# Kernel optimization log

Hardware: AMD Instinct MI355X
Metric: run time of the kernel (lower is better)

The kernel has to match this reference:

```python
import jax, jax.numpy as jnp
import numpy as np

NUM_HEADS = 16


def setup_inputs() -> dict:
    key = jax.random.key(0)
    k0, k1, k2, k3 = jax.random.split(key, 4)
    B, N, C = 8, 1024, 1024
    D = C // NUM_HEADS
    x = jax.random.normal(k0, (B, N, C), dtype=jnp.float32)
    # RoPE angle table [1, N, 1, head_dim]
    rope_freqs = jax.random.uniform(k1, (1, N, 1, D), dtype=jnp.float32) * (2.0 * jnp.pi)
    # qkv: Linear(dim, 3*dim, bias=False); proj: Linear(dim, dim) with bias
    qkv_w = jax.random.normal(k2, (3 * C, C), dtype=jnp.float32) * 0.02
    proj_w = jax.random.normal(k3, (C, C), dtype=jnp.float32) * 0.02
    proj_b = jnp.zeros((C,), dtype=jnp.float32)
    return {"x": x, "rope_freqs": rope_freqs, "qkv_w": qkv_w, "proj_w": proj_w, "proj_b": proj_b}


def _rotate_half(t):
    t1, t2 = jnp.split(t, 2, axis=-1)
    return jnp.concatenate([-t2, t1], axis=-1)


def reference(x, rope_freqs, qkv_w, proj_w, proj_b):
    B, N, C = x.shape
    H = NUM_HEADS
    D = C // H
    scale = D ** (-0.5)
    # QKV projection -> [3, B, H, N, D]
    qkv = (x @ qkv_w.T).reshape(B, N, 3, H, D).transpose(2, 0, 3, 1, 4)
    q, k, v = qkv[0], qkv[1], qkv[2]
    # RoPE: freqs [1, N, 1, D] -> [1, 1, N, D], applied to all tokens (n_special = 0)
    freqs = jnp.transpose(rope_freqs, (0, 2, 1, 3))
    cos = jnp.cos(freqs).astype(q.dtype)
    sin = jnp.sin(freqs).astype(q.dtype)
    q = q * cos + _rotate_half(q) * sin
    k = k * cos + _rotate_half(k) * sin
    # Full materialized attention (as in source)
    attn = jax.nn.softmax(jnp.einsum("bhnd,bhmd->bhnm", q, k) * scale, axis=-1)
    out = jnp.einsum("bhnm,bhmd->bhnd", attn, v)  # [B, H, N, D]
    out = out.transpose(0, 2, 1, 3).reshape(B, N, C)
    return out @ proj_w.T + proj_b
```

## Files before the change

kernel.cpp:

```cpp
#include <hip/hip_runtime.h>


typedef __attribute__((ext_vector_type(8))) short bf16x8;
typedef __attribute__((ext_vector_type(4))) float floatx4;
typedef __attribute__((ext_vector_type(4))) unsigned int u32x4;
typedef __attribute__((ext_vector_type(2))) unsigned int u32x2;

__device__ __forceinline__ void gld16(const void* g, void* l) {
  __builtin_amdgcn_global_load_lds((const __attribute__((address_space(1))) void*)g,
                                   (__attribute__((address_space(3))) void*)l, 16, 0, 0);
}

__device__ __forceinline__ short f2bf(float f) {
  unsigned u = __builtin_bit_cast(unsigned, f);
  u = (u + 0x7FFFu + ((u >> 16) & 1u)) >> 16;
  return (short)u;
}
__device__ __forceinline__ unsigned cvtpk(float lo, float hi) {
  unsigned r;
  asm("v_cvt_pk_bf16_f32 %0, %1, %2" : "=v"(r) : "v"(lo), "v"(hi));
  return r;
}
__device__ __forceinline__ float pexp(float x) {
  float r;
  asm("v_exp_f32 %0, %1" : "=v"(r) : "v"(x));
  return r;
}

__global__ __launch_bounds__(256) void prep_all(const float* __restrict__ sx,
                                                const float* __restrict__ sq,
                                                const float* __restrict__ sp,
                                                short* __restrict__ dst,
                                                const float* __restrict__ ropef,
                                                float2* __restrict__ tbl) {
  int bid = blockIdx.x;
  if (bid < 12288) {
    int i = bid * 256 + threadIdx.x;
    const float4* src;
    if (i < 2097152)      src = reinterpret_cast<const float4*>(sx) + i;
    else if (i < 2883584) src = reinterpret_cast<const float4*>(sq) + (i - 2097152);
    else                  src = reinterpret_cast<const float4*>(sp) + (i - 2883584);
    float4 v = *src;
    short4 o;
    o.x = f2bf(v.x); o.y = f2bf(v.y); o.z = f2bf(v.z); o.w = f2bf(v.w);
    reinterpret_cast<short4*>(dst)[i] = o;
  } else {
    int i = (bid - 12288) * 256 + threadIdx.x;
    float v = ropef[i];
    tbl[i] = make_float2(cosf(v), sinf(v));
  }
}

#define QSCALE 0.18033688011112042f

__device__ __forceinline__ void gemm_main(const short* __restrict__ A,
                                          const short* __restrict__ Bm,
                                          short* As, short* Bs,
                                          floatx4 (&acc)[2][4],
                                          int bx, int by) {
  const int tid = threadIdx.x;
  const int wid = tid >> 6, lane = tid & 63;
  const int g = lane >> 4, l15 = lane & 15;
  const int wr = wid >> 2, wc = wid & 3;
  const size_t trow = (size_t)by * 128, tcol = (size_t)bx * 256;
  floatx4 zero = {0.f, 0.f, 0.f, 0.f};
  #pragma unroll
  for (int i = 0; i < 2; ++i)
    #pragma unroll
    for (int j = 0; j < 4; ++j) acc[i][j] = zero;

  auto stage = [&](int buf, int k0) {
    {
      const int cb = wid * 64;
      const int c  = cb + lane;
      const int r  = c >> 3, s = c & 7;
      const int koff = k0 + ((s ^ (r & 7)) << 3);
      gld16(A + (trow + r) * 1024 + koff, As + buf * 8192 + (size_t)cb * 8);
    }
    #pragma unroll
    for (int i = 0; i < 2; ++i) {
      const int cb = (i * 16 + wid) * 64;
      const int c  = cb + lane;
      const int r  = c >> 3, s = c & 7;
      const int koff = k0 + ((s ^ (r & 7)) << 3);
      gld16(Bm + (tcol + r) * 1024 + koff, Bs + buf * 16384 + (size_t)cb * 8);
    }
  };

  stage(0, 0);
  __syncthreads();

  for (int t = 0; t < 16; ++t) {
    const int buf = t & 1;
    if (t < 15) stage(buf ^ 1, (t + 1) * 64);
    const short* Ab = As + buf * 8192;
    const short* Bb = Bs + buf * 16384;
    #pragma unroll
    for (int ks = 0; ks < 2; ++ks) {
      bf16x8 af[2], bfr[4];
      #pragma unroll
      for (int mi = 0; mi < 2; ++mi) {
        int row = wr * 32 + mi * 16 + l15;
        int ch  = (ks * 4 + g) ^ (row & 7);
        af[mi] = *reinterpret_cast<const bf16x8*>(Ab + row * 64 + ch * 8);
      }
      #pragma unroll
      for (int nt = 0; nt < 4; ++nt) {
        int row = wc * 64 + nt * 16 + l15;
        int ch  = (ks * 4 + g) ^ (row & 7);
        bfr[nt] = *reinterpret_cast<const bf16x8*>(Bb + row * 64 + ch * 8);
      }
      __builtin_amdgcn_s_setprio(1);
      #pragma unroll
      for (int mi = 0; mi < 2; ++mi)
        #pragma unroll
        for (int nt = 0; nt < 4; ++nt)
          acc[mi][nt] = __builtin_amdgcn_mfma_f32_16x16x32_bf16(af[mi], bfr[nt],
                                                                acc[mi][nt], 0, 0, 0);
      __builtin_amdgcn_s_setprio(0);
    }
    __syncthreads();
  }
}

__global__ __launch_bounds__(1024, 4) void gemm_qkv_k(const short* __restrict__ A,
                                                      const short* __restrict__ Bm,
                                                      const float2* __restrict__ tbl,
                                                      short* __restrict__ qo,
                                                      short* __restrict__ ko,
                                                      short* __restrict__ vt) {
  extern __shared__ __align__(16) short smem[];
  short* As = smem;
  short* Bs = smem + 16384;
  const int id  = blockIdx.y * 12 + blockIdx.x;
  const int sid = (id & 7) * 96 + (id >> 3);
  const int bx  = sid % 12, by = sid / 12;
  floatx4 acc[2][4];
  gemm_main(A, Bm, As, Bs, acc, bx, by);

  const int tid = threadIdx.x;
  const int wid = tid >> 6, lane = tid & 63;
  const int g = lane >> 4, l15 = lane & 15;
  const int wr = wid >> 2, wc = wid & 3;
  const int trow = by * 128, tcol = bx * 256;
  const int which = bx >> 2;

  if (which < 2) {
    short* dst = which == 0 ? qo : ko;
    const float sc = which == 0 ? QSCALE : 1.0f;
    #pragma unroll
    for (int nt = 0; nt < 2; ++nt) {
      int col = tcol + wc * 64 + nt * 16 + l15;
      int hc = col & 1023, h = hc >> 6, d1 = hc & 63;
      #pragma unroll
      for (int mi = 0; mi < 2; ++mi)
        #pragma unroll
        for (int r = 0; r < 4; ++r) {
          int rowg = trow + wr * 32 + mi * 16 + g * 4 + r;
          int b = rowg >> 10, n = rowg & 1023;
          float a1 = acc[mi][nt][r], a2 = acc[mi][nt + 2][r];
          float2 c1 = tbl[n * 64 + d1];
          float2 c2 = tbl[n * 64 + d1 + 32];
          float o1 = (a1 * c1.x - a2 * c1.y) * sc;
          float o2 = (a2 * c2.x + a1 * c2.y) * sc;
          size_t base = ((size_t)(b * 16 + h) * 1024 + n) * 64;
          dst[base + d1]      = f2bf(o1);
          dst[base + d1 + 32] = f2bf(o2);
        }
    }
  } else {
    #pragma unroll
    for (int nt = 0; nt < 4; ++nt) {
      int col = tcol + wc * 64 + nt * 16 + l15;
      int hc = col & 1023, h = hc >> 6, d = hc & 63;
      #pragma unroll
      for (int mi = 0; mi < 2; ++mi) {
        int rowg = trow + wr * 32 + mi * 16 + g * 4;
        int b = rowg >> 10, n0 = rowg & 1023;
        ushort4 pk;
        pk.x = (unsigned short)f2bf(acc[mi][nt][0]);
        pk.y = (unsigned short)f2bf(acc[mi][nt][1]);
        pk.z = (unsigned short)f2bf(acc[mi][nt][2]);
        pk.w = (unsigned short)f2bf(acc[mi][nt][3]);
        *reinterpret_cast<ushort4*>((unsigned short*)vt +
            ((size_t)(b * 16 + h) * 64 + d) * 1024 + n0) = pk;
      }
    }
  }
}

__global__ __launch_bounds__(1024, 4) void gemm_proj_k(const short* __restrict__ A,
                                                       const short* __restrict__ Bm,
                                                       const float* __restrict__ pb,
                                                       float* __restrict__ out) {
  extern __shared__ __align__(16) short smem[];
  short* As = smem;
  short* Bs = smem + 16384;
  const int id  = blockIdx.y * 4 + blockIdx.x;
  const int sid = (id & 7) * 32 + (id >> 3);
  const int bx  = sid % 4, by = sid / 4;
  floatx4 acc[2][4];
  gemm_main(A, Bm, As, Bs, acc, bx, by);

  const int tid = threadIdx.x;
  const int wid = tid >> 6, lane = tid & 63;
  const int g = lane >> 4, l15 = lane & 15;
  const int wr = wid >> 2, wc = wid & 3;
  const int trow = by * 128, tcol = bx * 256;
  #pragma unroll
  for (int nt = 0; nt < 4; ++nt) {
    int col = tcol + wc * 64 + nt * 16 + l15;
    float bias = pb[col];
    #pragma unroll
    for (int mi = 0; mi < 2; ++mi)
      #pragma unroll
      for (int r = 0; r < 4; ++r) {
        int rowg = trow + wr * 32 + mi * 16 + g * 4 + r;
        out[(size_t)rowg * 1024 + col] = acc[mi][nt][r] + bias;
      }
  }
}

__global__ __launch_bounds__(256) void attn_kernel(const short* __restrict__ qs,
                                                   const short* __restrict__ ksrc,
                                                   const short* __restrict__ vt,
                                                   short* __restrict__ aout) {
  __shared__ __align__(16) short Kl[3][64 * 64];
  __shared__ __align__(16) short Vl[3][64 * 64];

  const int tid = threadIdx.x, wid = tid >> 6, lane = tid & 63;
  const int g = lane >> 4, l15 = lane & 15;
  const int bh = blockIdx.x, q0 = blockIdx.y * 256;
  const size_t bhoff = (size_t)bh * 1024 * 64;
  const short* Kb = ksrc + bhoff;
  const short* Vb = vt + bhoff;
  const int slb = (lane & 48) + ((lane >> 4) << 2);

  const short* QpA = qs + bhoff + (size_t)(q0 + wid * 16 + l15) * 64 + g * 8;
  bf16x8 qA0 = *reinterpret_cast<const bf16x8*>(QpA);
  bf16x8 qA1 = *reinterpret_cast<const bf16x8*>(QpA + 32);
  bf16x8 qB0 = *reinterpret_cast<const bf16x8*>(QpA + 64 * 64);
  bf16x8 qB1 = *reinterpret_cast<const bf16x8*>(QpA + 64 * 64 + 32);
  bf16x8 qC0 = *reinterpret_cast<const bf16x8*>(QpA + 128 * 64);
  bf16x8 qC1 = *reinterpret_cast<const bf16x8*>(QpA + 128 * 64 + 32);
  bf16x8 qD0 = *reinterpret_cast<const bf16x8*>(QpA + 192 * 64);
  bf16x8 qD1 = *reinterpret_cast<const bf16x8*>(QpA + 192 * 64 + 32);

  floatx4 oA[4], oB[4], oC[4], oD[4];
  floatx4 zero = {0.f, 0.f, 0.f, 0.f};
  #pragma unroll
  for (int i = 0; i < 4; ++i) { oA[i] = zero; oB[i] = zero; oC[i] = zero; oD[i] = zero; }
  float lrunA = 0.f, lrunB = 0.f, lrunC = 0.f, lrunD = 0.f;

  auto stage = [&](int buf, int t) {
    #pragma unroll
    for (int i = 0; i < 2; ++i) {
      const int cb = (i * 4 + wid) * 64;
      const int c = cb + lane;
      const int r = c >> 3, s = c & 7;
      const int off = (s ^ (r & 7)) << 3;
      gld16(Kb + (size_t)(t * 64 + r) * 64 + off, &Kl[buf][cb * 8]);
      gld16(Vb + (size_t)r * 1024 + t * 64 + off, &Vl[buf][cb * 8]);
    }
  };

#define SOFTSLICE(s_, lrun, pa)                                                \
  do {                                                                         \
    float p0 = pexp(s_[0][0]), p1 = pexp(s_[0][1]);                            \
    float p2 = pexp(s_[0][2]), p3 = pexp(s_[0][3]);                            \
    float p4 = pexp(s_[1][0]), p5 = pexp(s_[1][1]);                            \
    float p6 = pexp(s_[1][2]), p7 = pexp(s_[1][3]);                            \
    lrun += ((p0 + p1) + (p2 + p3)) + ((p4 + p5) + (p6 + p7));                 \
    unsigned wa0 = cvtpk(p0, p1), wa1 = cvtpk(p2, p3);                         \
    unsigned wb0 = cvtpk(p4, p5), wb1 = cvtpk(p6, p7);                         \
    u32x2 y0 = __builtin_amdgcn_permlane32_swap(wa0, wb0, false, false);       \
    u32x2 z0 = __builtin_amdgcn_permlane16_swap(y0[0], y0[1], false, false);   \
    u32x2 y1 = __builtin_amdgcn_permlane32_swap(wa1, wb1, false, false);       \
    u32x2 z1 = __builtin_amdgcn_permlane16_swap(y1[0], y1[1], false, false);   \
    u32x4 aw = {z0[0], z1[0], z0[1], z1[1]};                                   \
    pa = __builtin_bit_cast(bf16x8, aw);                                       \
  } while (0)

#define QKSLICE(base, sA_, sB_, sC_, sD_)                                      \
  __builtin_amdgcn_s_setprio(1);                                               \
  _Pragma("unroll")                                                            \
  for (int kk = 0; kk < 2; ++kk) {                                             \
    int krow = (base + kk) * 16 + l15;                                         \
    int ch0 = (g ^ (krow & 7)) << 3, ch1 = ((4 + g) ^ (krow & 7)) << 3;        \
    bf16x8 kf0 = *reinterpret_cast<const bf16x8*>(&Kl[btop][krow * 64 + ch0]); \
    sA_[kk] = __builtin_amdgcn_mfma_f32_16x16x32_bf16(kf0, qA0, sA_[kk],0,0,0);\
    sB_[kk] = __builtin_amdgcn_mfma_f32_16x16x32_bf16(kf0, qB0, sB_[kk],0,0,0);\
    sC_[kk] = __builtin_amdgcn_mfma_f32_16x16x32_bf16(kf0, qC0, sC_[kk],0,0,0);\
    sD_[kk] = __builtin_amdgcn_mfma_f32_16x16x32_bf16(kf0, qD0, sD_[kk],0,0,0);\
    bf16x8 kf1 = *reinterpret_cast<const bf16x8*>(&Kl[btop][krow * 64 + ch1]); \
    sA_[kk] = __builtin_amdgcn_mfma_f32_16x16x32_bf16(kf1, qA1, sA_[kk],0,0,0);\
    sB_[kk] = __builtin_amdgcn_mfma_f32_16x16x32_bf16(kf1, qB1, sB_[kk],0,0,0);\
    sC_[kk] = __builtin_amdgcn_mfma_f32_16x16x32_bf16(kf1, qC1, sC_[kk],0,0,0);\
    sD_[kk] = __builtin_amdgcn_mfma_f32_16x16x32_bf16(kf1, qD1, sD_[kk],0,0,0);\
  }                                                                            \
  __builtin_amdgcn_s_setprio(0);

#define PVSLICE(chsel, paA_, paB_, paC_, paD_)                                 \
  __builtin_amdgcn_s_setprio(1);                                               \
  _Pragma("unroll")                                                            \
  for (int nt = 0; nt < 4; ++nt) {                                             \
    int row = nt * 16 + l15;                                                   \
    int ch = (((chsel) + g) ^ (row & 7)) << 3;                                 \
    bf16x8 vf = *reinterpret_cast<const bf16x8*>(&Vl[btop][row * 64 + ch]);    \
    oA[nt] = __builtin_amdgcn_mfma_f32_16x16x32_bf16(paA_, vf, oA[nt],0,0,0);  \
    oB[nt] = __builtin_amdgcn_mfma_f32_16x16x32_bf16(paB_, vf, oB[nt],0,0,0);  \
    oC[nt] = __builtin_amdgcn_mfma_f32_16x16x32_bf16(paC_, vf, oC[nt],0,0,0);  \
    oD[nt] = __builtin_amdgcn_mfma_f32_16x16x32_bf16(paD_, vf, oD[nt],0,0,0);  \
  }                                                                            \
  __builtin_amdgcn_s_setprio(0);

  stage(0, 0);
  stage(1, 1);
  asm volatile("s_waitcnt vmcnt(4)" ::: "memory");
  __builtin_amdgcn_s_barrier();
  asm volatile("" ::: "memory");

  int btop = 0;
  for (int t = 0; t < 16; ++t) {
    if (t < 14) {
      int bnx = btop + 2; if (bnx >= 3) bnx -= 3;
      stage(bnx, t + 2);
    }

    {
      floatx4 sA[2], sB[2], sC[2], sD[2];
      #pragma unroll
      for (int kk = 0; kk < 2; ++kk) { sA[kk]=zero; sB[kk]=zero; sC[kk]=zero; sD[kk]=zero; }
      QKSLICE(0, sA, sB, sC, sD);
      bf16x8 paA, paB, paC, paD;
      SOFTSLICE(sA, lrunA, paA);
      SOFTSLICE(sB, lrunB, paB);
      SOFTSLICE(sC, lrunC, paC);
      SOFTSLICE(sD, lrunD, paD);
      PVSLICE(0, paA, paB, paC, paD);
    }
    {
      floatx4 sA[2], sB[2], sC[2], sD[2];
      #pragma unroll
      for (int kk = 0; kk < 2; ++kk) { sA[kk]=zero; sB[kk]=zero; sC[kk]=zero; sD[kk]=zero; }
      QKSLICE(2, sA, sB, sC, sD);
      bf16x8 paA, paB, paC, paD;
      SOFTSLICE(sA, lrunA, paA);
      SOFTSLICE(sB, lrunB, paB);
      SOFTSLICE(sC, lrunC, paC);
      SOFTSLICE(sD, lrunD, paD);
      PVSLICE(4, paA, paB, paC, paD);
    }

    if (t < 15) {
      if (t < 14) asm volatile("s_waitcnt vmcnt(4)" ::: "memory");
      else        asm volatile("s_waitcnt vmcnt(0)" ::: "memory");
      __builtin_amdgcn_s_barrier();
      asm volatile("" ::: "memory");
    }
    btop = btop + 1 == 3 ? 0 : btop + 1;
  }

  const int b = bh >> 4, h = bh & 15;
  lrunA += __shfl_xor(lrunA, 16); lrunA += __shfl_xor(lrunA, 32);
  lrunB += __shfl_xor(lrunB, 16); lrunB += __shfl_xor(lrunB, 32);
  lrunC += __shfl_xor(lrunC, 16); lrunC += __shfl_xor(lrunC, 32);
  lrunD += __shfl_xor(lrunD, 16); lrunD += __shfl_xor(lrunD, 32);
  float invA = 1.f / lrunA, invB = 1.f / lrunB;
  float invC = 1.f / lrunC, invD = 1.f / lrunD;
  #pragma unroll
  for (int r = 0; r < 4; ++r) {
    float irA = __shfl(invA, slb + r);
    float irB = __shfl(invB, slb + r);
    float irC = __shfl(invC, slb + r);
    float irD = __shfl(invD, slb + r);
    int nA = q0 + wid * 16 + g * 4 + r;
    size_t baseA = ((size_t)(b * 1024) + nA) * 1024 + h * 64;
    size_t baseB = baseA + (size_t)64 * 1024;
    size_t baseC = baseA + (size_t)128 * 1024;
    size_t baseD = baseA + (size_t)192 * 1024;
    #pragma unroll
    for (int nt = 0; nt < 4; ++nt) {
      aout[baseA + nt * 16 + l15] = f2bf(oA[nt][r] * irA);
      aout[baseB + nt * 16 + l15] = f2bf(oB[nt][r] * irB);
      aout[baseC + nt * 16 + l15] = f2bf(oC[nt][r] * irC);
      aout[baseD + nt * 16 + l15] = f2bf(oD[nt][r] * irD);
    }
  }
#undef SOFTSLICE
#undef QKSLICE
#undef PVSLICE
}

extern "C" void kernel_launch(void* const* d_in, const int* in_sizes, int n_in,
                              void* d_out, int out_size, void* d_ws, size_t ws_size,
                              hipStream_t stream) {
  const float* x      = (const float*)d_in[0];
  const float* ropef  = (const float*)d_in[1];
  const float* qkv_w  = (const float*)d_in[2];
  const float* proj_w = (const float*)d_in[3];
  const float* proj_b = (const float*)d_in[4];
  float* out = (float*)d_out;

  char* ws = (char*)d_ws;
  short*  xb  = (short*)(ws + 0);
  short*  wqb = (short*)(ws + 16777216);
  short*  wpb = (short*)(ws + 23068672);
  short*  qb  = (short*)(ws + 25165824);
  short*  kb  = (short*)(ws + 41943040);
  short*  vtb = (short*)(ws + 58720256);
  short*  aob = (short*)(ws + 75497472);
  float2* tbl = (float2*)(ws + 92274688);

  prep_all<<<12544, 256, 0, stream>>>(x, qkv_w, proj_w, xb, ropef, tbl);

  gemm_qkv_k<<<dim3(12, 64), 1024, 98304, stream>>>(xb, wqb, tbl, qb, kb, vtb);
  attn_kernel<<<dim3(128, 4), 256, 0, stream>>>(qb, kb, vtb, aob);
  gemm_proj_k<<<dim3(4, 64), 1024, 98304, stream>>>(aob, wpb, proj_b, out);
}
```

Baseline: 156.1 us.

## Triple-buffer GEMM k-loop with 512-thread blocks and larger per-wave tiles

The shared GEMM mainloop moves from double to triple buffering, prefetching two k-stages ahead and replacing __syncthreads with explicit vmcnt waits plus s_barrier. Blocks shrink from 1024 to 512 threads, so each wave computes a 64x64 subtile with 16 accumulators instead of 8, and LDS grows to 144KB. The fp32-to-bf16 prep kernel becomes grid-stride with packed v_cvt_pk_bf16 conversions. The aim is better latency hiding and more operand reuse per wave, at the cost of more registers and LDS, which may reduce occupancy.

```diff
diff --git a/kernel.cpp b/kernel.cpp
--- a/kernel.cpp
+++ b/kernel.cpp
@@ -34,18 +34,20 @@
                                                 const float* __restrict__ ropef,
                                                 float2* __restrict__ tbl) {
   int bid = blockIdx.x;
-  if (bid < 12288) {
-    int i = bid * 256 + threadIdx.x;
-    const float4* src;
-    if (i < 2097152)      src = reinterpret_cast<const float4*>(sx) + i;
-    else if (i < 2883584) src = reinterpret_cast<const float4*>(sq) + (i - 2097152);
-    else                  src = reinterpret_cast<const float4*>(sp) + (i - 2883584);
-    float4 v = *src;
-    short4 o;
-    o.x = f2bf(v.x); o.y = f2bf(v.y); o.z = f2bf(v.z); o.w = f2bf(v.w);
-    reinterpret_cast<short4*>(dst)[i] = o;
+  if (bid < 2048) {
+    for (int i = bid * 256 + threadIdx.x; i < 3145728; i += 2048 * 256) {
+      const float4* src;
+      if (i < 2097152)      src = reinterpret_cast<const float4*>(sx) + i;
+      else if (i < 2883584) src = reinterpret_cast<const float4*>(sq) + (i - 2097152);
+      else                  src = reinterpret_cast<const float4*>(sp) + (i - 2883584);
+      float4 v = *src;
+      uint2 o;
+      o.x = cvtpk(v.x, v.y);
+      o.y = cvtpk(v.z, v.w);
+      reinterpret_cast<uint2*>(dst)[i] = o;
+    }
   } else {
-    int i = (bid - 12288) * 256 + threadIdx.x;
+    int i = (bid - 2048) * 256 + threadIdx.x;
     float v = ropef[i];
     tbl[i] = make_float2(cosf(v), sinf(v));
   }
@@ -56,7 +58,7 @@
 __device__ __forceinline__ void gemm_main(const short* __restrict__ A,
                                           const short* __restrict__ Bm,
                                           short* As, short* Bs,
-                                          floatx4 (&acc)[2][4],
+                                          floatx4 (&acc)[4][4],
                                           int bx, int by) {
   const int tid = threadIdx.x;
   const int wid = tid >> 6, lane = tid & 63;
@@ -65,21 +67,22 @@
   const size_t trow = (size_t)by * 128, tcol = (size_t)bx * 256;
   floatx4 zero = {0.f, 0.f, 0.f, 0.f};
   #pragma unroll
-  for (int i = 0; i < 2; ++i)
+  for (int i = 0; i < 4; ++i)
     #pragma unroll
     for (int j = 0; j < 4; ++j) acc[i][j] = zero;
 
   auto stage = [&](int buf, int k0) {
-    {
-      const int cb = wid * 64;
+    #pragma unroll
+    for (int i = 0; i < 2; ++i) {
+      const int cb = (i * 8 + wid) * 64;
       const int c  = cb + lane;
       const int r  = c >> 3, s = c & 7;
       const int koff = k0 + ((s ^ (r & 7)) << 3);
       gld16(A + (trow + r) * 1024 + koff, As + buf * 8192 + (size_t)cb * 8);
     }
     #pragma unroll
-    for (int i = 0; i < 2; ++i) {
-      const int cb = (i * 16 + wid) * 64;
+    for (int i = 0; i < 4; ++i) {
+      const int cb = (i * 8 + wid) * 64;
       const int c  = cb + lane;
       const int r  = c >> 3, s = c & 7;
       const int koff = k0 + ((s ^ (r & 7)) << 3);
@@ -88,19 +91,25 @@
   };
 
   stage(0, 0);
-  __syncthreads();
-
+  stage(1, 64);
+  asm volatile("s_waitcnt vmcnt(6)" ::: "memory");
+  __builtin_amdgcn_s_barrier();
+  asm volatile("" ::: "memory");
+
+  int btop = 0;
   for (int t = 0; t < 16; ++t) {
-    const int buf = t & 1;
-    if (t < 15) stage(buf ^ 1, (t + 1) * 64);
-    const short* Ab = As + buf * 8192;
-    const short* Bb = Bs + buf * 16384;
+    if (t < 14) {
+      int bnx = btop + 2; if (bnx >= 3) bnx -= 3;
+      stage(bnx, (t + 2) * 64);
+    }
+    const short* Ab = As + btop * 8192;
+    const short* Bb = Bs + btop * 16384;
     #pragma unroll
     for (int ks = 0; ks < 2; ++ks) {
-      bf16x8 af[2], bfr[4];
-      #pragma unroll
-      for (int mi = 0; mi < 2; ++mi) {
-        int row = wr * 32 + mi * 16 + l15;
+      bf16x8 af[4], bfr[4];
+      #pragma unroll
+      for (int mi = 0; mi < 4; ++mi) {
+        int row = wr * 64 + mi * 16 + l15;
         int ch  = (ks * 4 + g) ^ (row & 7);
         af[mi] = *reinterpret_cast<const bf16x8*>(Ab + row * 64 + ch * 8);
       }
@@ -112,30 +121,36 @@
       }
       __builtin_amdgcn_s_setprio(1);
       #pragma unroll
-      for (int mi = 0; mi < 2; ++mi)
+      for (int mi = 0; mi < 4; ++mi)
         #pragma unroll
         for (int nt = 0; nt < 4; ++nt)
           acc[mi][nt] = __builtin_amdgcn_mfma_f32_16x16x32_bf16(af[mi], bfr[nt],
                                                                 acc[mi][nt], 0, 0, 0);
       __builtin_amdgcn_s_setprio(0);
     }
-    __syncthreads();
-  }
-}
-
-__global__ __launch_bounds__(1024, 4) void gemm_qkv_k(const short* __restrict__ A,
-                                                      const short* __restrict__ Bm,
-                                                      const float2* __restrict__ tbl,
-                                                      short* __restrict__ qo,
-                                                      short* __restrict__ ko,
-                                                      short* __restrict__ vt) {
+    if (t < 15) {
+      if (t < 14) asm volatile("s_waitcnt vmcnt(6)" ::: "memory");
+      else        asm volatile("s_waitcnt vmcnt(0)" ::: "memory");
+      __builtin_amdgcn_s_barrier();
+      asm volatile("" ::: "memory");
+    }
+    btop = btop + 1 == 3 ? 0 : btop + 1;
+  }
+}
+
+__global__ __launch_bounds__(512) void gemm_qkv_k(const short* __restrict__ A,
+                                                  const short* __restrict__ Bm,
+                                                  const float2* __restrict__ tbl,
+                                                  short* __restrict__ qo,
+                                                  short* __restrict__ ko,
+                                                  short* __restrict__ vt) {
   extern __shared__ __align__(16) short smem[];
   short* As = smem;
-  short* Bs = smem + 16384;
+  short* Bs = smem + 24576;
   const int id  = blockIdx.y * 12 + blockIdx.x;
   const int sid = (id & 7) * 96 + (id >> 3);
   const int bx  = sid % 12, by = sid / 12;
-  floatx4 acc[2][4];
+  floatx4 acc[4][4];
   gemm_main(A, Bm, As, Bs, acc, bx, by);
 
   const int tid = threadIdx.x;
@@ -153,10 +168,10 @@
       int col = tcol + wc * 64 + nt * 16 + l15;
       int hc = col & 1023, h = hc >> 6, d1 = hc & 63;
       #pragma unroll
-      for (int mi = 0; mi < 2; ++mi)
+      for (int mi = 0; mi < 4; ++mi)
         #pragma unroll
         for (int r = 0; r < 4; ++r) {
-          int rowg = trow + wr * 32 + mi * 16 + g * 4 + r;
+          int rowg = trow + wr * 64 + mi * 16 + g * 4 + r;
           int b = rowg >> 10, n = rowg & 1023;
           float a1 = acc[mi][nt][r], a2 = acc[mi][nt + 2][r];
           float2 c1 = tbl[n * 64 + d1];
@@ -174,8 +189,8 @@
       int col = tcol + wc * 64 + nt * 16 + l15;
       int hc = col & 1023, h = hc >> 6, d = hc & 63;
       #pragma unroll
-      for (int mi = 0; mi < 2; ++mi) {
-        int rowg = trow + wr * 32 + mi * 16 + g * 4;
+      for (int mi = 0; mi < 4; ++mi) {
+        int rowg = trow + wr * 64 + mi * 16 + g * 4;
         int b = rowg >> 10, n0 = rowg & 1023;
         ushort4 pk;
         pk.x = (unsigned short)f2bf(acc[mi][nt][0]);
@@ -189,17 +204,17 @@
   }
 }
 
-__global__ __launch_bounds__(1024, 4) void gemm_proj_k(const short* __restrict__ A,
-                                                       const short* __restrict__ Bm,
-                                                       const float* __restrict__ pb,
-                                                       float* __restrict__ out) {
+__global__ __launch_bounds__(512) void gemm_proj_k(const short* __restrict__ A,
+                                                   const short* __restrict__ Bm,
+                                                   const float* __restrict__ pb,
+                                                   float* __restrict__ out) {
   extern __shared__ __align__(16) short smem[];
   short* As = smem;
-  short* Bs = smem + 16384;
+  short* Bs = smem + 24576;
   const int id  = blockIdx.y * 4 + blockIdx.x;
   const int sid = (id & 7) * 32 + (id >> 3);
   const int bx  = sid % 4, by = sid / 4;
-  floatx4 acc[2][4];
+  floatx4 acc[4][4];
   gemm_main(A, Bm, As, Bs, acc, bx, by);
 
   const int tid = threadIdx.x;
@@ -212,10 +227,10 @@
     int col = tcol + wc * 64 + nt * 16 + l15;
     float bias = pb[col];
     #pragma unroll
-    for (int mi = 0; mi < 2; ++mi)
+    for (int mi = 0; mi < 4; ++mi)
       #pragma unroll
       for (int r = 0; r < 4; ++r) {
-        int rowg = trow + wr * 32 + mi * 16 + g * 4 + r;
+        int rowg = trow + wr * 64 + mi * 16 + g * 4 + r;
         out[(size_t)rowg * 1024 + col] = acc[mi][nt][r] + bias;
       }
   }
@@ -412,9 +427,9 @@
   short*  aob = (short*)(ws + 75497472);
   float2* tbl = (float2*)(ws + 92274688);
 
-  prep_all<<<12544, 256, 0, stream>>>(x, qkv_w, proj_w, xb, ropef, tbl);
-
-  gemm_qkv_k<<<dim3(12, 64), 1024, 98304, stream>>>(xb, wqb, tbl, qb, kb, vtb);
+  prep_all<<<2304, 256, 0, stream>>>(x, qkv_w, proj_w, xb, ropef, tbl);
+
+  gemm_qkv_k<<<dim3(12, 64), 512, 147456, stream>>>(xb, wqb, tbl, qb, kb, vtb);
   attn_kernel<<<dim3(128, 4), 256, 0, stream>>>(qb, kb, vtb, aob);
-  gemm_proj_k<<<dim3(4, 64), 1024, 98304, stream>>>(aob, wpb, proj_b, out);
-}
+  gemm_proj_k<<<dim3(4, 64), 512, 147456, stream>>>(aob, wpb, proj_b, out);
+}
```

New measurement: 159.9 us. 2.4% more time.
